# Kernel tuning notes

Measured on AMD Instinct MI355X. Metric: run time of the kernel, lower is better.

## Reference

```python
import jax, jax.numpy as jnp
import numpy as np

S, N, H, E, V, K = 128, 256, 1024, 512, 32000, 1024  # seq, batch, hidden, embed, vocab, energy channels


def setup_inputs() -> dict:
    key = jax.random.key(0)
    ks = jax.random.split(key, 10)
    s = 0.02
    return {
        "input": jax.random.randint(ks[0], (N,), 0, V),
        "encoder_states": jax.random.normal(ks[1], (S, N, H), jnp.float32),
        "hidden": jax.random.normal(ks[2], (1, N, H), jnp.float32),
        "cell": jax.random.normal(ks[3], (1, N, H), jnp.float32),
        "emb": jax.random.normal(ks[4], (V, E), jnp.float32) * s,
        "W_energy": jax.random.normal(ks[5], (K, 2 * H), jnp.float32) * s,
        "b_energy": jnp.zeros((K,), jnp.float32),
        "W_ih": jax.random.normal(ks[6], (4 * H, H + E), jnp.float32) * s,
        "b_ih": jnp.zeros((4 * H,), jnp.float32),
        "W_hh": jax.random.normal(ks[7], (4 * H, H), jnp.float32) * s,
        "b_hh": jnp.zeros((4 * H,), jnp.float32),
        "W_fc": jax.random.normal(ks[8], (V, H), jnp.float32) * s,
        "b_fc": jnp.zeros((V,), jnp.float32),
    }


def reference(input, encoder_states, hidden, cell, emb, W_energy, b_energy,
              W_ih, b_ih, W_hh, b_hh, W_fc, b_fc):
    seq = encoder_states.shape[0]
    n = encoder_states.shape[1]
    h0 = hidden[0]                                   # [N,H]
    c0 = cell[0]                                     # [N,H]
    emb_x = emb[input]                               # [N,E]

    # additive-attention energy: cat(hidden repeated over S, encoder_states) -> Linear -> ReLU
    h_rep = jnp.broadcast_to(hidden, (seq, n, hidden.shape[2]))
    cat = jnp.concatenate([h_rep, encoder_states], axis=2)          # [S,N,2H]
    energy = jax.nn.relu(jnp.einsum('snh,kh->snk', cat, W_energy) + b_energy)  # [S,N,K]
    # softmax over dim 0 (sequence), independently per (n,k) channel
    attn_last = jax.nn.softmax(energy[..., -1], axis=0)             # [S,N]
    # einsum('snk,snl->knl')[-1] only uses channel k=K-1; contract just that slice
    ctx = jnp.einsum('sn,snl->nl', attn_last, encoder_states)       # [N,H]

    # single-step LSTM (PyTorch gate order i,f,g,o)
    rnn_in = jnp.concatenate([ctx, emb_x], axis=1)                  # [N,H+E]
    gates = rnn_in @ W_ih.T + b_ih + h0 @ W_hh.T + b_hh             # [N,4H]
    i, f, g, o = jnp.split(gates, 4, axis=1)
    c1 = jax.nn.sigmoid(f) * c0 + jax.nn.sigmoid(i) * jnp.tanh(g)
    h1 = jax.nn.sigmoid(o) * jnp.tanh(c1)

    predictions = h1 @ W_fc.T + b_fc                                # [N,V]
    return predictions, h1[None], c1[None]
```

## Files before the change

kernel.cpp:

```cpp
#include <hip/hip_runtime.h>

#define S_DIM 128
#define N_DIM 256
#define H_DIM 1024
#define E_DIM 512
#define V_DIM 32000
#define KE_DIM 1024
#define CIN 2560
#define G4 4096

typedef unsigned short u16;
typedef __bf16 bf16x8 __attribute__((ext_vector_type(8)));
typedef float  f32x4  __attribute__((ext_vector_type(4)));

union U16x8 { uint4 u; bf16x8 b; };

__device__ __forceinline__ unsigned f2bf(float x) {
  unsigned u = __float_as_uint(x);
  return (u + 0x7FFFu + ((u >> 16) & 1u)) >> 16;
}
__device__ __forceinline__ unsigned pk2(float a, float b) {
  return f2bf(a) | (f2bf(b) << 16);
}

__device__ __forceinline__ bf16x8 frag_from_global(const u16* p) {
  U16x8 t; t.u = *(const uint4*)p; return t.b;
}
__device__ __forceinline__ bf16x8 frag_from_lds(const u16* base, int byteoff) {
  U16x8 t; t.u = *(const uint4*)((const char*)base + byteoff); return t.b;
}

__device__ __forceinline__ int loff64(int row, int k) {
  return row * 128 + ((((k >> 3) ^ (row & 7)) << 4) | ((k & 7) << 1));
}
__device__ __forceinline__ int loff128(int row, int k) {
  return row * 256 + ((((k >> 3) ^ (row & 7)) << 4) | ((k & 7) << 1));
}

__device__ __forceinline__ f32x4 mfma16(bf16x8 a, bf16x8 b, f32x4 c) {
  return __builtin_amdgcn_mfma_f32_16x16x32_bf16(a, b, c, 0, 0, 0);
}

__global__ __launch_bounds__(256) void k1_attn(
    const float* __restrict__ enc, const float* __restrict__ hid,
    const float* __restrict__ Wen, const float* __restrict__ ben,
    const int* __restrict__ inp, const float* __restrict__ emb,
    u16* __restrict__ A2)
{
  __shared__ float s_acc[4][H_DIM];
  __shared__ float s_ml[8];
  const int n = blockIdx.x;
  const int t = threadIdx.x;
  const int wave = t >> 6, lane = t & 63;

  const float* Wrow = Wen + (KE_DIM - 1) * (2 * H_DIM);
  float4 we[4];
  #pragma unroll
  for (int ks = 0; ks < 4; ++ks)
    we[ks] = *(const float4*)(Wrow + H_DIM + ks * 256 + lane * 4);

  float hd = 0.f;
  #pragma unroll
  for (int ks = 0; ks < 4; ++ks) {
    float4 wh = *(const float4*)(Wrow + ks * 256 + lane * 4);
    float4 hv = *(const float4*)(hid + n * H_DIM + ks * 256 + lane * 4);
    hd += wh.x * hv.x + wh.y * hv.y + wh.z * hv.z + wh.w * hv.w;
  }
  #pragma unroll
  for (int off = 32; off > 0; off >>= 1) hd += __shfl_xor(hd, off, 64);
  const float ebase = hd + ben[KE_DIM - 1];

  float m = -INFINITY, l = 0.f;
  float4 acc[4];
  #pragma unroll
  for (int ks = 0; ks < 4; ++ks) acc[ks] = make_float4(0.f, 0.f, 0.f, 0.f);

  const long rstride = 4L * N_DIM * H_DIM;
  const float* p = enc + ((long)wave * N_DIM + n) * H_DIM + lane * 4;
  float4 cur[4];
  #pragma unroll
  for (int ks = 0; ks < 4; ++ks) cur[ks] = *(const float4*)(p + ks * 256);

  for (int s = wave; s < S_DIM; s += 4) {
    float4 nxt[4];
    const float* pn = p + rstride;
    const bool has = (s + 4 < S_DIM);
    if (has) {
      #pragma unroll
      for (int ks = 0; ks < 4; ++ks) nxt[ks] = *(const float4*)(pn + ks * 256);
    }
    float d = 0.f;
    #pragma unroll
    for (int ks = 0; ks < 4; ++ks)
      d += we[ks].x * cur[ks].x + we[ks].y * cur[ks].y +
           we[ks].z * cur[ks].z + we[ks].w * cur[ks].w;
    #pragma unroll
    for (int off = 32; off > 0; off >>= 1) d += __shfl_xor(d, off, 64);
    const float e  = fmaxf(ebase + d, 0.f);
    const float nm = fmaxf(m, e);
    const float sc = __expf(m - nm);
    const float pe = __expf(e - nm);
    l = l * sc + pe;
    #pragma unroll
    for (int ks = 0; ks < 4; ++ks) {
      acc[ks].x = acc[ks].x * sc + pe * cur[ks].x;
      acc[ks].y = acc[ks].y * sc + pe * cur[ks].y;
      acc[ks].z = acc[ks].z * sc + pe * cur[ks].z;
      acc[ks].w = acc[ks].w * sc + pe * cur[ks].w;
    }
    m = nm;
    if (has) {
      #pragma unroll
      for (int ks = 0; ks < 4; ++ks) cur[ks] = nxt[ks];
    }
    p = pn;
  }

  #pragma unroll
  for (int ks = 0; ks < 4; ++ks)
    *(float4*)&s_acc[wave][ks * 256 + lane * 4] = acc[ks];
  if (lane == 0) { s_ml[wave] = m; s_ml[4 + wave] = l; }
  __syncthreads();

  const float M = fmaxf(fmaxf(s_ml[0], s_ml[1]), fmaxf(s_ml[2], s_ml[3]));
  const float f0 = __expf(s_ml[0] - M), f1 = __expf(s_ml[1] - M);
  const float f2 = __expf(s_ml[2] - M), f3 = __expf(s_ml[3] - M);
  const float L = s_ml[4] * f0 + s_ml[5] * f1 + s_ml[6] * f2 + s_ml[7] * f3;
  const float invL = 1.0f / L;
  {
    const int e0 = t * 4;
    float v0 = (s_acc[0][e0+0]*f0 + s_acc[1][e0+0]*f1 + s_acc[2][e0+0]*f2 + s_acc[3][e0+0]*f3) * invL;
    float v1 = (s_acc[0][e0+1]*f0 + s_acc[1][e0+1]*f1 + s_acc[2][e0+1]*f2 + s_acc[3][e0+1]*f3) * invL;
    float v2 = (s_acc[0][e0+2]*f0 + s_acc[1][e0+2]*f1 + s_acc[2][e0+2]*f2 + s_acc[3][e0+2]*f3) * invL;
    float v3 = (s_acc[0][e0+3]*f0 + s_acc[1][e0+3]*f1 + s_acc[2][e0+3]*f2 + s_acc[3][e0+3]*f3) * invL;
    uint2 pk; pk.x = pk2(v0, v1); pk.y = pk2(v2, v3);
    *(uint2*)&A2[(long)n * CIN + e0] = pk;
  }

  const int idx = inp[n];
  for (int j = t; j < E_DIM + H_DIM; j += 256) {
    float v = (j < E_DIM) ? emb[(long)idx * E_DIM + j]
                          : hid[n * H_DIM + (j - E_DIM)];
    A2[(long)n * CIN + H_DIM + j] = (u16)f2bf(v);
  }
}

__global__ __launch_bounds__(256) void k2_gates(
    const u16* __restrict__ A2, const float* __restrict__ Wih,
    const float* __restrict__ bih, const float* __restrict__ Whh,
    const float* __restrict__ bhh, float* __restrict__ gates)
{
  __shared__ u16 Blds[16 * 128];
  const int t = threadIdx.x;
  const int wave = t >> 6, lane = t & 63;
  const int quad = lane >> 4, l15 = lane & 15;
  const int j0 = blockIdx.x * 16;
  const int br = t >> 4;
  const int bk = (t & 15) * 8;

  f32x4 acc[4];
  #pragma unroll
  for (int mt = 0; mt < 4; ++mt) acc[mt] = (f32x4){0.f, 0.f, 0.f, 0.f};

  const float* s0 = Wih + (long)(j0 + br) * 1536 + bk;
  float4 v0 = *(const float4*)s0;
  float4 v1 = *(const float4*)(s0 + 4);

  for (int kt = 0; kt < 20; ++kt) {
    const int k0 = kt * 128;
    uint4 pk;
    pk.x = pk2(v0.x, v0.y); pk.y = pk2(v0.z, v0.w);
    pk.z = pk2(v1.x, v1.y); pk.w = pk2(v1.z, v1.w);
    *(uint4*)((char*)Blds + loff128(br, bk)) = pk;
    if (kt + 1 < 20) {
      const int kn = k0 + 128 + bk;
      const float* sn = (kn < 1536) ? (Wih + (long)(j0 + br) * 1536 + kn)
                                    : (Whh + (long)(j0 + br) * 1024 + (kn - 1536));
      v0 = *(const float4*)sn;
      v1 = *(const float4*)(sn + 4);
    }
    __syncthreads();
    #pragma unroll
    for (int kstep = 0; kstep < 4; ++kstep) {
      const int kl = kstep * 32 + quad * 8;
      const bf16x8 bfrag = frag_from_lds(Blds, loff128(l15, kl));
      #pragma unroll
      for (int mt = 0; mt < 4; ++mt) {
        const int row = wave * 64 + mt * 16 + l15;
        const bf16x8 afrag = frag_from_global(A2 + (long)row * CIN + k0 + kl);
        acc[mt] = mfma16(afrag, bfrag, acc[mt]);
      }
    }
    __syncthreads();
  }

  const float bias = bih[j0 + l15] + bhh[j0 + l15];
  #pragma unroll
  for (int mt = 0; mt < 4; ++mt) {
    #pragma unroll
    for (int r = 0; r < 4; ++r) {
      const int row = wave * 64 + mt * 16 + quad * 4 + r;
      gates[(long)row * G4 + j0 + l15] = acc[mt][r] + bias;
    }
  }
}

__global__ __launch_bounds__(256) void k2b_lstm(
    const float* __restrict__ gates, const float* __restrict__ cell,
    float* __restrict__ h1, float* __restrict__ c1, u16* __restrict__ h1b)
{
  const int i = blockIdx.x * 256 + threadIdx.x;
  const int n = i >> 10, h = i & 1023;
  const float* g = gates + (long)n * G4 + h;
  const float gi = g[0], gf = g[1024], gg = g[2048], go = g[3072];
  const float si = 1.f / (1.f + __expf(-gi));
  const float sf = 1.f / (1.f + __expf(-gf));
  const float so = 1.f / (1.f + __expf(-go));
  const float tg = tanhf(gg);
  const float cv = sf * cell[i] + si * tg;
  const float hv = so * tanhf(cv);
  c1[i] = cv;
  h1[i] = hv;
  h1b[i] = (u16)f2bf(hv);
}

__global__ __launch_bounds__(256) void k3_fc(
    const u16* __restrict__ h1b, const float* __restrict__ Wfc,
    const float* __restrict__ bfc, float* __restrict__ out)
{
  __shared__ u16 Blds[64 * 64];
  const int t = threadIdx.x;
  const int wave = t >> 6, lane = t & 63;
  const int quad = lane >> 4, l15 = lane & 15;
  const int j0 = blockIdx.x * 64;
  const int br = t >> 2;
  const int bk = (t & 3) * 16;
  const float* bsrc = Wfc + (long)(j0 + br) * 1024 + bk;

  f32x4 acc[4][4];
  #pragma unroll
  for (int mt = 0; mt < 4; ++mt)
    #pragma unroll
    for (int nt = 0; nt < 4; ++nt) acc[mt][nt] = (f32x4){0.f, 0.f, 0.f, 0.f};

  float4 v0 = *(const float4*)(bsrc);
  float4 v1 = *(const float4*)(bsrc + 4);
  float4 v2 = *(const float4*)(bsrc + 8);
  float4 v3 = *(const float4*)(bsrc + 12);

  for (int kt = 0; kt < 16; ++kt) {
    const int k0 = kt * 64;
    uint4 pa, pb;
    pa.x = pk2(v0.x, v0.y); pa.y = pk2(v0.z, v0.w);
    pa.z = pk2(v1.x, v1.y); pa.w = pk2(v1.z, v1.w);
    pb.x = pk2(v2.x, v2.y); pb.y = pk2(v2.z, v2.w);
    pb.z = pk2(v3.x, v3.y); pb.w = pk2(v3.z, v3.w);
    *(uint4*)((char*)Blds + loff64(br, bk)) = pa;
    *(uint4*)((char*)Blds + loff64(br, bk + 8)) = pb;
    if (kt + 1 < 16) {
      const float* sn = bsrc + (k0 + 64);
      v0 = *(const float4*)(sn);
      v1 = *(const float4*)(sn + 4);
      v2 = *(const float4*)(sn + 8);
      v3 = *(const float4*)(sn + 12);
    }
    __syncthreads();
    #pragma unroll
    for (int kstep = 0; kstep < 2; ++kstep) {
      const int kl = kstep * 32 + quad * 8;
      bf16x8 bfrag[4], afrag[4];
      #pragma unroll
      for (int nt = 0; nt < 4; ++nt)
        bfrag[nt] = frag_from_lds(Blds, loff64(nt * 16 + l15, kl));
      #pragma unroll
      for (int mt = 0; mt < 4; ++mt)
        afrag[mt] = frag_from_global(h1b + (long)(wave * 64 + mt * 16 + l15) * 1024 + k0 + kl);
      #pragma unroll
      for (int mt = 0; mt < 4; ++mt)
        #pragma unroll
        for (int nt = 0; nt < 4; ++nt)
          acc[mt][nt] = mfma16(afrag[mt], bfrag[nt], acc[mt][nt]);
    }
    __syncthreads();
  }

  #pragma unroll
  for (int nt = 0; nt < 4; ++nt) {
    const float bv = bfc[j0 + nt * 16 + l15];
    #pragma unroll
    for (int mt = 0; mt < 4; ++mt) {
      #pragma unroll
      for (int r = 0; r < 4; ++r) {
        const int row = wave * 64 + mt * 16 + quad * 4 + r;
        out[(long)row * V_DIM + j0 + nt * 16 + l15] = acc[mt][nt][r] + bv;
      }
    }
  }
}

extern "C" void kernel_launch(void* const* d_in, const int* in_sizes, int n_in,
                              void* d_out, int out_size, void* d_ws, size_t ws_size,
                              hipStream_t stream) {
  const int*   inp  = (const int*)  d_in[0];
  const float* enc  = (const float*)d_in[1];
  const float* hid  = (const float*)d_in[2];
  const float* cell = (const float*)d_in[3];
  const float* emb  = (const float*)d_in[4];
  const float* Wen  = (const float*)d_in[5];
  const float* ben  = (const float*)d_in[6];
  const float* Wih  = (const float*)d_in[7];
  const float* bih  = (const float*)d_in[8];
  const float* Whh  = (const float*)d_in[9];
  const float* bhh  = (const float*)d_in[10];
  const float* Wfc  = (const float*)d_in[11];
  const float* bfc  = (const float*)d_in[12];

  float* out  = (float*)d_out;
  float* pred = out;
  float* h1   = out + (long)N_DIM * V_DIM;
  float* c1   = h1 + (long)N_DIM * H_DIM;

  char* ws = (char*)d_ws;
  u16*   A2    = (u16*)ws;
  float* gates = (float*)(ws + 1310720);
  u16*   h1b   = (u16*)(ws + 1310720 + 4194304);

  k1_attn <<<N_DIM,            256, 0, stream>>>(enc, hid, Wen, ben, inp, emb, A2);
  k2_gates<<<G4 / 16,          256, 0, stream>>>(A2, Wih, bih, Whh, bhh, gates);
  k2b_lstm<<<(N_DIM*H_DIM)/256,256, 0, stream>>>(gates, cell, h1, c1, h1b);
  k3_fc   <<<V_DIM / 64,       256, 0, stream>>>(h1b, Wfc, bfc, pred);
}
```

Baseline: 425.8 us.

## Fuse LSTM pointwise into gates GEMM, widen attention block, deepen FC k-tile

The LSTM gate columns are remapped so each gates block owns the i,f,g,o rows for four hidden units, which lets the sigmoid/tanh cell update run in the GEMM epilogue through shared memory. This removes the separate pointwise kernel and the global gates buffer round trip. The attention kernel now uses 8 waves per batch row to put more loads in flight, and the FC kernel stages 128-wide k tiles to halve its barrier count. In exchange there is more shared memory and register pressure per block.

```diff
diff --git a/kernel.cpp b/kernel.cpp
--- a/kernel.cpp
+++ b/kernel.cpp
@@ -7,7 +7,6 @@
 #define V_DIM 32000
 #define KE_DIM 1024
 #define CIN 2560
-#define G4 4096
 
 typedef unsigned short u16;
 typedef __bf16 bf16x8 __attribute__((ext_vector_type(8)));
@@ -30,9 +29,6 @@
   U16x8 t; t.u = *(const uint4*)((const char*)base + byteoff); return t.b;
 }
 
-__device__ __forceinline__ int loff64(int row, int k) {
-  return row * 128 + ((((k >> 3) ^ (row & 7)) << 4) | ((k & 7) << 1));
-}
 __device__ __forceinline__ int loff128(int row, int k) {
   return row * 256 + ((((k >> 3) ^ (row & 7)) << 4) | ((k & 7) << 1));
 }
@@ -41,14 +37,14 @@
   return __builtin_amdgcn_mfma_f32_16x16x32_bf16(a, b, c, 0, 0, 0);
 }
 
-__global__ __launch_bounds__(256) void k1_attn(
+__global__ __launch_bounds__(512) void k1_attn(
     const float* __restrict__ enc, const float* __restrict__ hid,
     const float* __restrict__ Wen, const float* __restrict__ ben,
     const int* __restrict__ inp, const float* __restrict__ emb,
     u16* __restrict__ A2)
 {
-  __shared__ float s_acc[4][H_DIM];
-  __shared__ float s_ml[8];
+  __shared__ float s_acc[8][H_DIM];
+  __shared__ float s_ml[16];
   const int n = blockIdx.x;
   const int t = threadIdx.x;
   const int wave = t >> 6, lane = t & 63;
@@ -75,16 +71,16 @@
   #pragma unroll
   for (int ks = 0; ks < 4; ++ks) acc[ks] = make_float4(0.f, 0.f, 0.f, 0.f);
 
-  const long rstride = 4L * N_DIM * H_DIM;
+  const long rstride = 8L * N_DIM * H_DIM;
   const float* p = enc + ((long)wave * N_DIM + n) * H_DIM + lane * 4;
   float4 cur[4];
   #pragma unroll
   for (int ks = 0; ks < 4; ++ks) cur[ks] = *(const float4*)(p + ks * 256);
 
-  for (int s = wave; s < S_DIM; s += 4) {
+  for (int s = wave; s < S_DIM; s += 8) {
     float4 nxt[4];
     const float* pn = p + rstride;
-    const bool has = (s + 4 < S_DIM);
+    const bool has = (s + 8 < S_DIM);
     if (has) {
       #pragma unroll
       for (int ks = 0; ks < 4; ++ks) nxt[ks] = *(const float4*)(pn + ks * 256);
@@ -119,26 +115,29 @@
   #pragma unroll
   for (int ks = 0; ks < 4; ++ks)
     *(float4*)&s_acc[wave][ks * 256 + lane * 4] = acc[ks];
-  if (lane == 0) { s_ml[wave] = m; s_ml[4 + wave] = l; }
+  if (lane == 0) { s_ml[wave] = m; s_ml[8 + wave] = l; }
   __syncthreads();
 
-  const float M = fmaxf(fmaxf(s_ml[0], s_ml[1]), fmaxf(s_ml[2], s_ml[3]));
-  const float f0 = __expf(s_ml[0] - M), f1 = __expf(s_ml[1] - M);
-  const float f2 = __expf(s_ml[2] - M), f3 = __expf(s_ml[3] - M);
-  const float L = s_ml[4] * f0 + s_ml[5] * f1 + s_ml[6] * f2 + s_ml[7] * f3;
+  float M = s_ml[0];
+  #pragma unroll
+  for (int w = 1; w < 8; ++w) M = fmaxf(M, s_ml[w]);
+  float f[8]; float L = 0.f;
+  #pragma unroll
+  for (int w = 0; w < 8; ++w) { f[w] = __expf(s_ml[w] - M); L += s_ml[8 + w] * f[w]; }
   const float invL = 1.0f / L;
   {
-    const int e0 = t * 4;
-    float v0 = (s_acc[0][e0+0]*f0 + s_acc[1][e0+0]*f1 + s_acc[2][e0+0]*f2 + s_acc[3][e0+0]*f3) * invL;
-    float v1 = (s_acc[0][e0+1]*f0 + s_acc[1][e0+1]*f1 + s_acc[2][e0+1]*f2 + s_acc[3][e0+1]*f3) * invL;
-    float v2 = (s_acc[0][e0+2]*f0 + s_acc[1][e0+2]*f1 + s_acc[2][e0+2]*f2 + s_acc[3][e0+2]*f3) * invL;
-    float v3 = (s_acc[0][e0+3]*f0 + s_acc[1][e0+3]*f1 + s_acc[2][e0+3]*f2 + s_acc[3][e0+3]*f3) * invL;
-    uint2 pk; pk.x = pk2(v0, v1); pk.y = pk2(v2, v3);
-    *(uint2*)&A2[(long)n * CIN + e0] = pk;
+    const int e0 = t * 2;
+    float v0 = 0.f, v1 = 0.f;
+    #pragma unroll
+    for (int w = 0; w < 8; ++w) {
+      v0 += s_acc[w][e0]     * f[w];
+      v1 += s_acc[w][e0 + 1] * f[w];
+    }
+    *(unsigned*)&A2[(long)n * CIN + e0] = pk2(v0 * invL, v1 * invL);
   }
 
   const int idx = inp[n];
-  for (int j = t; j < E_DIM + H_DIM; j += 256) {
+  for (int j = t; j < E_DIM + H_DIM; j += 512) {
     float v = (j < E_DIM) ? emb[(long)idx * E_DIM + j]
                           : hid[n * H_DIM + (j - E_DIM)];
     A2[(long)n * CIN + H_DIM + j] = (u16)f2bf(v);
@@ -148,21 +147,24 @@
 __global__ __launch_bounds__(256) void k2_gates(
     const u16* __restrict__ A2, const float* __restrict__ Wih,
     const float* __restrict__ bih, const float* __restrict__ Whh,
-    const float* __restrict__ bhh, float* __restrict__ gates)
+    const float* __restrict__ bhh, const float* __restrict__ cell0,
+    float* __restrict__ h1, float* __restrict__ c1, u16* __restrict__ h1b)
 {
   __shared__ u16 Blds[16 * 128];
+  __shared__ float sg[256][17];
   const int t = threadIdx.x;
   const int wave = t >> 6, lane = t & 63;
   const int quad = lane >> 4, l15 = lane & 15;
-  const int j0 = blockIdx.x * 16;
+  const int b = blockIdx.x;
   const int br = t >> 4;
   const int bk = (t & 15) * 8;
+  const int jbr = (br >> 2) * H_DIM + b * 4 + (br & 3);
 
   f32x4 acc[4];
   #pragma unroll
   for (int mt = 0; mt < 4; ++mt) acc[mt] = (f32x4){0.f, 0.f, 0.f, 0.f};
 
-  const float* s0 = Wih + (long)(j0 + br) * 1536 + bk;
+  const float* s0 = Wih + (long)jbr * 1536 + bk;
   float4 v0 = *(const float4*)s0;
   float4 v1 = *(const float4*)(s0 + 4);
 
@@ -174,8 +176,8 @@
     *(uint4*)((char*)Blds + loff128(br, bk)) = pk;
     if (kt + 1 < 20) {
       const int kn = k0 + 128 + bk;
-      const float* sn = (kn < 1536) ? (Wih + (long)(j0 + br) * 1536 + kn)
-                                    : (Whh + (long)(j0 + br) * 1024 + (kn - 1536));
+      const float* sn = (kn < 1536) ? (Wih + (long)jbr * 1536 + kn)
+                                    : (Whh + (long)jbr * H_DIM + (kn - 1536));
       v0 = *(const float4*)sn;
       v1 = *(const float4*)(sn + 4);
     }
@@ -194,48 +196,47 @@
     __syncthreads();
   }
 
-  const float bias = bih[j0 + l15] + bhh[j0 + l15];
-  #pragma unroll
-  for (int mt = 0; mt < 4; ++mt) {
-    #pragma unroll
-    for (int r = 0; r < 4; ++r) {
-      const int row = wave * 64 + mt * 16 + quad * 4 + r;
-      gates[(long)row * G4 + j0 + l15] = acc[mt][r] + bias;
-    }
-  }
-}
-
-__global__ __launch_bounds__(256) void k2b_lstm(
-    const float* __restrict__ gates, const float* __restrict__ cell,
-    float* __restrict__ h1, float* __restrict__ c1, u16* __restrict__ h1b)
-{
-  const int i = blockIdx.x * 256 + threadIdx.x;
-  const int n = i >> 10, h = i & 1023;
-  const float* g = gates + (long)n * G4 + h;
-  const float gi = g[0], gf = g[1024], gg = g[2048], go = g[3072];
-  const float si = 1.f / (1.f + __expf(-gi));
-  const float sf = 1.f / (1.f + __expf(-gf));
-  const float so = 1.f / (1.f + __expf(-go));
-  const float tg = tanhf(gg);
-  const float cv = sf * cell[i] + si * tg;
-  const float hv = so * tanhf(cv);
-  c1[i] = cv;
-  h1[i] = hv;
-  h1b[i] = (u16)f2bf(hv);
+  {
+    const int jj = (l15 >> 2) * H_DIM + b * 4 + (l15 & 3);
+    const float bias = bih[jj] + bhh[jj];
+    #pragma unroll
+    for (int mt = 0; mt < 4; ++mt)
+      #pragma unroll
+      for (int r = 0; r < 4; ++r)
+        sg[wave * 64 + mt * 16 + quad * 4 + r][l15] = acc[mt][r] + bias;
+  }
+  __syncthreads();
+
+  #pragma unroll
+  for (int u = 0; u < 4; ++u) {
+    const int id = t + u * 256;
+    const int n = id >> 2, q = id & 3, h = b * 4 + q;
+    const float gi = sg[n][q],      gf = sg[n][4 + q];
+    const float gg = sg[n][8 + q],  go = sg[n][12 + q];
+    const float si = 1.f / (1.f + __expf(-gi));
+    const float sf = 1.f / (1.f + __expf(-gf));
+    const float so = 1.f / (1.f + __expf(-go));
+    const float tg = tanhf(gg);
+    const float cv = sf * cell0[(long)n * H_DIM + h] + si * tg;
+    const float hv = so * tanhf(cv);
+    c1 [(long)n * H_DIM + h] = cv;
+    h1 [(long)n * H_DIM + h] = hv;
+    h1b[(long)n * H_DIM + h] = (u16)f2bf(hv);
+  }
 }
 
 __global__ __launch_bounds__(256) void k3_fc(
     const u16* __restrict__ h1b, const float* __restrict__ Wfc,
     const float* __restrict__ bfc, float* __restrict__ out)
 {
-  __shared__ u16 Blds[64 * 64];
+  __shared__ u16 Blds[64 * 128];
   const int t = threadIdx.x;
   const int wave = t >> 6, lane = t & 63;
   const int quad = lane >> 4, l15 = lane & 15;
   const int j0 = blockIdx.x * 64;
   const int br = t >> 2;
-  const int bk = (t & 3) * 16;
-  const float* bsrc = Wfc + (long)(j0 + br) * 1024 + bk;
+  const int bk = (t & 3) * 32;
+  const float* bsrc = Wfc + (long)(j0 + br) * H_DIM + bk;
 
   f32x4 acc[4][4];
   #pragma unroll
@@ -243,38 +244,35 @@
     #pragma unroll
     for (int nt = 0; nt < 4; ++nt) acc[mt][nt] = (f32x4){0.f, 0.f, 0.f, 0.f};
 
-  float4 v0 = *(const float4*)(bsrc);
-  float4 v1 = *(const float4*)(bsrc + 4);
-  float4 v2 = *(const float4*)(bsrc + 8);
-  float4 v3 = *(const float4*)(bsrc + 12);
-
-  for (int kt = 0; kt < 16; ++kt) {
-    const int k0 = kt * 64;
-    uint4 pa, pb;
-    pa.x = pk2(v0.x, v0.y); pa.y = pk2(v0.z, v0.w);
-    pa.z = pk2(v1.x, v1.y); pa.w = pk2(v1.z, v1.w);
-    pb.x = pk2(v2.x, v2.y); pb.y = pk2(v2.z, v2.w);
-    pb.z = pk2(v3.x, v3.y); pb.w = pk2(v3.z, v3.w);
-    *(uint4*)((char*)Blds + loff64(br, bk)) = pa;
-    *(uint4*)((char*)Blds + loff64(br, bk + 8)) = pb;
-    if (kt + 1 < 16) {
-      const float* sn = bsrc + (k0 + 64);
-      v0 = *(const float4*)(sn);
-      v1 = *(const float4*)(sn + 4);
-      v2 = *(const float4*)(sn + 8);
-      v3 = *(const float4*)(sn + 12);
+  float4 v[8];
+  #pragma unroll
+  for (int i = 0; i < 8; ++i) v[i] = *(const float4*)(bsrc + 4 * i);
+
+  for (int kt = 0; kt < 8; ++kt) {
+    const int k0 = kt * 128;
+    #pragma unroll
+    for (int i = 0; i < 4; ++i) {
+      uint4 pk;
+      pk.x = pk2(v[2*i].x, v[2*i].y); pk.y = pk2(v[2*i].z, v[2*i].w);
+      pk.z = pk2(v[2*i+1].x, v[2*i+1].y); pk.w = pk2(v[2*i+1].z, v[2*i+1].w);
+      *(uint4*)((char*)Blds + loff128(br, bk + 8 * i)) = pk;
+    }
+    if (kt + 1 < 8) {
+      const float* sn = bsrc + (k0 + 128);
+      #pragma unroll
+      for (int i = 0; i < 8; ++i) v[i] = *(const float4*)(sn + 4 * i);
     }
     __syncthreads();
     #pragma unroll
-    for (int kstep = 0; kstep < 2; ++kstep) {
+    for (int kstep = 0; kstep < 4; ++kstep) {
       const int kl = kstep * 32 + quad * 8;
       bf16x8 bfrag[4], afrag[4];
       #pragma unroll
       for (int nt = 0; nt < 4; ++nt)
-        bfrag[nt] = frag_from_lds(Blds, loff64(nt * 16 + l15, kl));
+        bfrag[nt] = frag_from_lds(Blds, loff128(nt * 16 + l15, kl));
       #pragma unroll
       for (int mt = 0; mt < 4; ++mt)
-        afrag[mt] = frag_from_global(h1b + (long)(wave * 64 + mt * 16 + l15) * 1024 + k0 + kl);
+        afrag[mt] = frag_from_global(h1b + (long)(wave * 64 + mt * 16 + l15) * H_DIM + k0 + kl);
       #pragma unroll
       for (int mt = 0; mt < 4; ++mt)
         #pragma unroll
@@ -304,7 +302,7 @@
   const int*   inp  = (const int*)  d_in[0];
   const float* enc  = (const float*)d_in[1];
   const float* hid  = (const float*)d_in[2];
-  const float* cell = (const float*)d_in[3];
+  const float* cel  = (const float*)d_in[3];
   const float* emb  = (const float*)d_in[4];
   const float* Wen  = (const float*)d_in[5];
   const float* ben  = (const float*)d_in[6];
@@ -321,12 +319,10 @@
   float* c1   = h1 + (long)N_DIM * H_DIM;
 
   char* ws = (char*)d_ws;
-  u16*   A2    = (u16*)ws;
-  float* gates = (float*)(ws + 1310720);
-  u16*   h1b   = (u16*)(ws + 1310720 + 4194304);
-
-  k1_attn <<<N_DIM,            256, 0, stream>>>(enc, hid, Wen, ben, inp, emb, A2);
-  k2_gates<<<G4 / 16,          256, 0, stream>>>(A2, Wih, bih, Whh, bhh, gates);
-  k2b_lstm<<<(N_DIM*H_DIM)/256,256, 0, stream>>>(gates, cell, h1, c1, h1b);
-  k3_fc   <<<V_DIM / 64,       256, 0, stream>>>(h1b, Wfc, bfc, pred);
-}
+  u16* A2  = (u16*)ws;
+  u16* h1b = (u16*)(ws + 1310720);
+
+  k1_attn <<<N_DIM,    512, 0, stream>>>(enc, hid, Wen, ben, inp, emb, A2);
+  k2_gates<<<N_DIM,    256, 0, stream>>>(A2, Wih, bih, Whh, bhh, cel, h1, c1, h1b);
+  k3_fc   <<<V_DIM/64, 256, 0, stream>>>(h1b, Wfc, bfc, pred);
+}
```

After: 422.8 us. Within noise of the previous version (-0.7%).
